# Kernel optimization log

Hardware: AMD Instinct MI355X
Metric: run time of the kernel (lower is better)

Reference implementation:

```python
import jax, jax.numpy as jnp
import numpy as np

EMBED_DIM = 768
NUM_HEADS = 12
HEAD_DIM = EMBED_DIM // NUM_HEADS
BSZ = 8
N_NODE = 512


def setup_inputs() -> dict:
    key = jax.random.key(0)
    ks = jax.random.split(key, 12)
    s = 0.02
    E = EMBED_DIM
    return {
        "query": jax.random.normal(ks[0], (N_NODE, BSZ, E), jnp.float32),
        "attention_bias": jax.random.normal(ks[1], (BSZ, NUM_HEADS, N_NODE, N_NODE), jnp.float32),
        "node_position": jax.random.normal(ks[2], (BSZ, N_NODE, 3), jnp.float32),
        "Wq": jax.random.normal(ks[3], (E, E), jnp.float32) * s,
        "bq": jnp.zeros((E,), jnp.float32),
        "Wk": jax.random.normal(ks[4], (E, E), jnp.float32) * s,
        "bk": jnp.zeros((E,), jnp.float32),
        "Wv": jax.random.normal(ks[5], (E, E), jnp.float32) * s,
        "bv": jnp.zeros((E,), jnp.float32),
        "W1": jax.random.normal(ks[6], (E, 1), jnp.float32) * s,
        "b1": jnp.zeros((1,), jnp.float32),
        "W2": jax.random.normal(ks[7], (E, 1), jnp.float32) * s,
        "b2": jnp.zeros((1,), jnp.float32),
        "W3": jax.random.normal(ks[8], (E, 1), jnp.float32) * s,
        "b3": jnp.zeros((1,), jnp.float32),
    }


def reference(query, attention_bias, node_position, Wq, bq, Wk, bk, Wv, bv,
              W1, b1, W2, b2, W3, b3):
    bsz, n = node_position.shape[:2]
    H = attention_bias.shape[1]
    E = query.shape[-1]
    hd = E // H
    scaling = hd ** -0.5

    # unit direction vectors between node pairs: delta[b,i,j] = pos[j]-pos[i]
    delta = node_position[:, None, :, :] - node_position[:, :, None, :]  # (b,n,n,3)
    dist = jnp.linalg.norm(delta, axis=-1)                               # (b,n,n)
    delta = delta / (dist[..., None] + 1e-5)

    x = jnp.swapaxes(query, 0, 1)  # (b,n,E)
    q = (x @ Wq + bq).reshape(bsz, n, H, hd).transpose(0, 2, 1, 3) * scaling  # (b,h,n,d)
    k = (x @ Wk + bk).reshape(bsz, n, H, hd).transpose(0, 2, 1, 3)
    v = (x @ Wv + bv).reshape(bsz, n, H, hd).transpose(0, 2, 1, 3)

    attn = jnp.einsum('bhid,bhjd->bhij', q, k)
    probs = jax.nn.softmax(attn + attention_bias, axis=-1)  # (b,h,i,j); dropout = identity (eval)

    # rotational aggregation: out[b,i,c,h,d] = sum_j probs[b,h,i,j]*delta[b,i,j,c]*v[b,h,j,d]
    xo = jnp.einsum('bhij,bijc,bhjd->bichd', probs, delta, v).reshape(bsz, n, 3, E)

    f1 = xo[:, :, 0, :] @ W1 + b1  # (b,n,1)
    f2 = xo[:, :, 1, :] @ W2 + b2
    f3 = xo[:, :, 2, :] @ W3 + b3
    return jnp.concatenate([f1, f2, f3], axis=-1).astype(jnp.float32)  # (b,n,3)
```

## Files before the change

kernel.cpp:

```cpp
#include <hip/hip_runtime.h>
#include <math.h>

#define EDIM 768
#define NH 12
#define HD 64
#define BSZ 8
#define NN 512
#define NCAT 1664

typedef short short8 __attribute__((ext_vector_type(8)));
typedef float f32x4 __attribute__((ext_vector_type(4)));

__device__ __forceinline__ unsigned short f2bf(float x) {
    unsigned int u = __float_as_uint(x);
    u = (u + 0x7FFF + ((u >> 16) & 1)) >> 16;
    return (unsigned short)u;
}
__device__ __forceinline__ float bf2f(unsigned short s) {
    return __uint_as_float(((unsigned int)s) << 16);
}
__device__ __forceinline__ void gl2lds16(const void* g, void* l) {
    __builtin_amdgcn_global_load_lds(
        (const __attribute__((address_space(1))) unsigned int*)g,
        (__attribute__((address_space(3))) unsigned int*)l, 16, 0, 0);
}

#define PB_GEOM_END 512
#define PB_TR_END   1664
#define PB_VW_END   1772
#define PB_CVT_END  3308
#define PB_BC_END   3315
#define PREP_BLOCKS 3350

__global__ __launch_bounds__(256) void k_prep(
        const float* __restrict__ query, const float* __restrict__ pos,
        const float* __restrict__ Wq, const float* __restrict__ bq,
        const float* __restrict__ Wk, const float* __restrict__ bk,
        const float* __restrict__ Wv, const float* __restrict__ bv,
        const float* __restrict__ W1, const float* __restrict__ W2,
        const float* __restrict__ W3,
        unsigned short* __restrict__ WT, float* __restrict__ bcat,
        unsigned short* __restrict__ Xb,
        unsigned int* __restrict__ udp) {
    __shared__ float sm[1536];
    const int bid = blockIdx.x;
    const int t = threadIdx.x;

    if (bid < PB_GEOM_END) {
        float* psx = sm; float* psy = sm + NN; float* psz = sm + 2 * NN;
        const int b = bid >> 6, i0 = (bid & 63) * 8;
        for (int idx = t; idx < NN; idx += 256) {
            const float* p = pos + ((size_t)b * NN + idx) * 3;
            psx[idx] = p[0]; psy[idx] = p[1]; psz[idx] = p[2];
        }
        __syncthreads();
        const int i = i0 + (t >> 5);
        const float qx = psx[i], qy = psy[i], qz = psz[i];
        const size_t row = ((size_t)b * NN + i) * NN;
        for (int jt = 0; jt < 4; jt++) {
            int j = ((t & 31) + jt * 32) * 4;
            unsigned int s0[4], s1[4], s2[4];
            #pragma unroll
            for (int u = 0; u < 4; u++) {
                float dx = psx[j + u] - qx, dy = psy[j + u] - qy, dz = psz[j + u] - qz;
                float inv = 1.f / (sqrtf(dx * dx + dy * dy + dz * dz) + 1e-5f);
                s0[u] = f2bf(dx * inv); s1[u] = f2bf(dy * inv); s2[u] = f2bf(dz * inv);
            }
            uint4 A = {s0[0] | (s1[0] << 16), s2[0], s0[1] | (s1[1] << 16), s2[1]};
            uint4 B = {s0[2] | (s1[2] << 16), s2[2], s0[3] | (s1[3] << 16), s2[3]};
            *(uint4*)&udp[(row + j) * 2]     = A;
            *(uint4*)&udp[(row + j) * 2 + 4] = B;
        }
    } else if (bid < PB_TR_END) {
        float (*tile)[33] = (float(*)[33])sm;
        const int tb = bid - PB_GEOM_END;
        const int n0 = (tb % 48) * 32, e0 = (tb / 48) * 32;
        const float* src = (n0 < 768) ? Wq : Wk;
        const int ol0 = (n0 < 768) ? n0 : (n0 - 768);
        const int tx = t & 31, ty = t >> 5;
        #pragma unroll
        for (int s = 0; s < 4; s++)
            tile[ty + s * 8][tx] = src[(size_t)(e0 + ty + s * 8) * EDIM + ol0 + tx];
        __syncthreads();
        #pragma unroll
        for (int s = 0; s < 4; s++)
            WT[(size_t)(n0 + ty + s * 8) * EDIM + e0 + tx] = f2bf(tile[tx][ty + s * 8]);
    } else if (bid < PB_VW_END) {
        int idx = (bid - PB_TR_END) * 256 + t;
        int o2 = idx / 768, e = idx - o2 * 768;
        int h = o2 / 3, c = o2 - (o2 / 3) * 3;
        const float* Wc = (c == 0) ? W1 : (c == 1) ? W2 : W3;
        const float4* wvp = (const float4*)(Wv + (size_t)e * EDIM + h * HD);
        const float4* wcp = (const float4*)(Wc + h * HD);
        float s = 0.f;
        #pragma unroll
        for (int d4 = 0; d4 < 16; d4++) {
            float4 a = wvp[d4], b = wcp[d4];
            s += a.x * b.x + a.y * b.y + a.z * b.z + a.w * b.w;
        }
        WT[(size_t)(1536 + o2) * EDIM + e] = f2bf(s);
    } else if (bid < PB_CVT_END) {
        int idx = (bid - PB_VW_END) * 256 + t;
        int m = idx / 96, e8 = (idx - (idx / 96) * 96) * 8;
        int b = m >> 9, i = m & (NN - 1);
        const float* src = query + ((size_t)i * BSZ + b) * EDIM + e8;
        float4 v0 = *(const float4*)src;
        float4 v1 = *(const float4*)(src + 4);
        unsigned int p0 = f2bf(v0.x) | ((unsigned int)f2bf(v0.y) << 16);
        unsigned int p1 = f2bf(v0.z) | ((unsigned int)f2bf(v0.w) << 16);
        unsigned int p2 = f2bf(v1.x) | ((unsigned int)f2bf(v1.y) << 16);
        unsigned int p3 = f2bf(v1.z) | ((unsigned int)f2bf(v1.w) << 16);
        uint4 pk = {p0, p1, p2, p3};
        *(uint4*)&Xb[(size_t)idx * 8] = pk;
    } else if (bid < PB_BC_END) {
        int o = (bid - PB_CVT_END) * 256 + t;
        if (o < NCAT) {
            float v = 0.f;
            if (o < 768) v = bq[o];
            else if (o < 1536) v = bk[o - 768];
            else if (o < 1572) {
                int o2 = o - 1536;
                int h = o2 / 3, c = o2 - (o2 / 3) * 3;
                const float* Wc = (c == 0) ? W1 : (c == 1) ? W2 : W3;
                float s = 0.f;
                for (int d = 0; d < HD; d++) s += bv[h * HD + d] * Wc[h * HD + d];
                v = s;
            }
            bcat[o] = v;
        }
    } else {
        int tid = (bid - PB_BC_END) * 256 + t;
        if (tid < 8832) {
            uint4 z = {0, 0, 0, 0};
            *(uint4*)&WT[(size_t)1572 * EDIM + (size_t)tid * 8] = z;
        }
    }
}

__global__ __launch_bounds__(256) void k_gemm_qkv(
        const unsigned short* __restrict__ Xb, const unsigned short* __restrict__ WT,
        const float* __restrict__ bcat,
        unsigned short* __restrict__ qb, unsigned short* __restrict__ kb,
        float* __restrict__ vwb) {
    __shared__ short As[8 * 64 * 8];
    __shared__ short Bs[8 * 128 * 8];
    const int t = threadIdx.x;
    const int m0 = blockIdx.x * 64, n0 = blockIdx.y * 128;
    const int w = t >> 6, lane = t & 63, quad = lane >> 4, ln = lane & 15;
    const int wm = (w & 1) * 32, wn = (w >> 1) * 64;

    f32x4 acc[2][4];
    #pragma unroll
    for (int mi = 0; mi < 2; mi++)
        #pragma unroll
        for (int ni = 0; ni < 4; ni++) acc[mi][ni] = (f32x4){0.f, 0.f, 0.f, 0.f};

    for (int k0 = 0; k0 < EDIM; k0 += 64) {
        __syncthreads();
        #pragma unroll
        for (int is = 0; is < 2; is++) {
            int slot = is * 256 + t;
            int g = slot >> 6, m = slot & 63;
            gl2lds16(Xb + (size_t)(m0 + m) * EDIM + k0 + g * 8, &As[(size_t)(is * 256 + w * 64) * 8]);
        }
        #pragma unroll
        for (int is = 0; is < 4; is++) {
            int slot = is * 256 + t;
            int g = slot >> 7, n = slot & 127;
            gl2lds16(WT + (size_t)(n0 + n) * EDIM + k0 + g * 8, &Bs[(size_t)(is * 256 + w * 64) * 8]);
        }
        __syncthreads();
        #pragma unroll
        for (int s = 0; s < 2; s++) {
            short8 af[2], bf[4];
            #pragma unroll
            for (int mi = 0; mi < 2; mi++)
                af[mi] = *(const short8*)&As[(size_t)((s * 4 + quad) * 64 + wm + mi * 16 + ln) * 8];
            #pragma unroll
            for (int ni = 0; ni < 4; ni++)
                bf[ni] = *(const short8*)&Bs[(size_t)((s * 4 + quad) * 128 + wn + ni * 16 + ln) * 8];
            #pragma unroll
            for (int mi = 0; mi < 2; mi++)
                #pragma unroll
                for (int ni = 0; ni < 4; ni++)
                    acc[mi][ni] = __builtin_amdgcn_mfma_f32_16x16x32_bf16(af[mi], bf[ni], acc[mi][ni], 0, 0, 0);
        }
    }

    #pragma unroll
    for (int mi = 0; mi < 2; mi++) {
        #pragma unroll
        for (int r = 0; r < 4; r++) {
            int mg = m0 + wm + mi * 16 + quad * 4 + r;
            int b_ = mg >> 9, i_ = mg & (NN - 1);
            #pragma unroll
            for (int ni = 0; ni < 4; ni++) {
                int o = n0 + wn + ni * 16 + ln;
                float val = acc[mi][ni][r] + bcat[o];
                if (o < 768) {
                    int h = o >> 6, d = o & 63;
                    qb[(((size_t)b_ * NH + h) * NN + i_) * HD + d] = f2bf(val * 0.125f);
                } else if (o < 1536) {
                    int o2 = o - 768;
                    int h = o2 >> 6, d = o2 & 63;
                    kb[(((size_t)b_ * NH + h) * NN + i_) * HD + d] = f2bf(val);
                } else if (o < 1572) {
                    int o2 = o - 1536;
                    int h = o2 / 3, c = o2 - (o2 / 3) * 3;
                    vwb[(((size_t)b_ * NH + h) * NN + i_) * 3 + c] = val;
                }
            }
        }
    }
}

__global__ __launch_bounds__(256, 4) void k_attn(
        const unsigned short* __restrict__ qb, const unsigned short* __restrict__ kb,
        const float* __restrict__ vwb, const float* __restrict__ bias,
        const unsigned int* __restrict__ udp,
        float* __restrict__ mp, float* __restrict__ lp,
        float* __restrict__ a0p, float* __restrict__ a1p, float* __restrict__ a2p) {
    __shared__ uint4 Qs[64 * 8];
    __shared__ uint4 Ks[128 * 8];
    __shared__ float ws0[128], ws1[128], ws2[128];

    const int t = threadIdx.x;
    const int bid = blockIdx.x;
    const int h = bid % NH;
    const int r1 = bid / NH;
    const int js = r1 & 3;
    const int it = (r1 >> 2) & 7;
    const int b = r1 >> 5;
    const int i0 = it * 64;
    const int jb = js * 128;
    const int w = t >> 6, lane = t & 63, quad = lane >> 4, ln = lane & 15;
    const size_t bh = (size_t)b * NH + h;

    const uint4* qg = (const uint4*)(qb + (bh * NN + i0) * HD);
    const uint4* kg = (const uint4*)(kb + (bh * NN + jb) * HD);
    const int rr = t >> 3, cc = t & 7;
    uint4 qv0 = qg[t];
    uint4 qv1 = qg[256 + t];
    uint4 kv0 = kg[t];
    uint4 kv1 = kg[256 + t];
    uint4 kv2 = kg[512 + t];
    uint4 kv3 = kg[768 + t];
    float wv0 = vwb[bh * (NN * 3) + (size_t)jb * 3 + t];
    float wv1 = (t < 128) ? vwb[bh * (NN * 3) + (size_t)jb * 3 + 256 + t] : 0.f;

    const float* bbase = bias + (bh * NN + i0 + w * 16 + quad * 4) * NN + jb + ln;
    f32x4 acc[8];
    #pragma unroll
    for (int jsub = 0; jsub < 8; jsub++)
        #pragma unroll
        for (int r = 0; r < 4; r++)
            acc[jsub][r] = bbase[r * NN + jsub * 16];

    const int sw = cc ^ (rr & 7);
    Qs[rr * 8 + sw] = qv0;
    Qs[(rr + 32) * 8 + sw] = qv1;
    Ks[rr * 8 + sw] = kv0;
    Ks[(rr + 32) * 8 + sw] = kv1;
    Ks[(rr + 64) * 8 + sw] = kv2;
    Ks[(rr + 96) * 8 + sw] = kv3;
    {
        int jj = t / 3, c = t - (t / 3) * 3;
        if (c == 0) ws0[jj] = wv0; else if (c == 1) ws1[jj] = wv0; else ws2[jj] = wv0;
        if (t < 128) {
            int t2 = 256 + t;
            int jj2 = t2 / 3, c2 = t2 - (t2 / 3) * 3;
            if (c2 == 0) ws0[jj2] = wv1; else if (c2 == 1) ws1[jj2] = wv1; else ws2[jj2] = wv1;
        }
    }
    __syncthreads();

    const int qrow = w * 16 + ln;
    short8 a0f = *(const short8*)&Qs[qrow * 8 + (quad ^ (qrow & 7))];
    short8 a1f = *(const short8*)&Qs[qrow * 8 + ((quad + 4) ^ (qrow & 7))];
    #pragma unroll
    for (int jsub = 0; jsub < 8; jsub++) {
        int krow = jsub * 16 + ln;
        short8 b0f = *(const short8*)&Ks[krow * 8 + (quad ^ (krow & 7))];
        short8 b1f = *(const short8*)&Ks[krow * 8 + ((quad + 4) ^ (krow & 7))];
        acc[jsub] = __builtin_amdgcn_mfma_f32_16x16x32_bf16(a0f, b0f, acc[jsub], 0, 0, 0);
        acc[jsub] = __builtin_amdgcn_mfma_f32_16x16x32_bf16(a1f, b1f, acc[jsub], 0, 0, 0);
    }

    float m_r = acc[0][0];
    #pragma unroll
    for (int jsub = 0; jsub < 8; jsub++)
        #pragma unroll
        for (int r = 0; r < 4; r++) m_r = fmaxf(m_r, acc[jsub][r]);
    #pragma unroll
    for (int off = 1; off < 64; off <<= 1) m_r = fmaxf(m_r, __shfl_xor(m_r, off, 64));

    const unsigned int* udbase = udp + (((size_t)b * NN + i0 + w * 16 + quad * 4) * NN + jb + ln) * 2;
    float lr[4] = {0.f, 0.f, 0.f, 0.f};
    float A0[4] = {0.f, 0.f, 0.f, 0.f};
    float A1[4] = {0.f, 0.f, 0.f, 0.f};
    float A2[4] = {0.f, 0.f, 0.f, 0.f};
    #pragma unroll
    for (int jsub = 0; jsub < 8; jsub++) {
        float w0 = ws0[jsub * 16 + ln];
        float w1 = ws1[jsub * 16 + ln];
        float w2 = ws2[jsub * 16 + ln];
        #pragma unroll
        for (int r = 0; r < 4; r++) {
            uint2 U = *(const uint2*)&udbase[((size_t)r * NN + jsub * 16) * 2];
            float p = __expf(acc[jsub][r] - m_r);
            lr[r] += p;
            A0[r] = fmaf(p * bf2f((unsigned short)(U.x & 0xFFFF)), w0, A0[r]);
            A1[r] = fmaf(p * bf2f((unsigned short)(U.x >> 16)), w1, A1[r]);
            A2[r] = fmaf(p * bf2f((unsigned short)(U.y & 0xFFFF)), w2, A2[r]);
        }
    }

    #pragma unroll
    for (int off = 1; off < 16; off <<= 1) {
        #pragma unroll
        for (int r = 0; r < 4; r++) {
            lr[r] += __shfl_xor(lr[r], off, 64);
            A0[r] += __shfl_xor(A0[r], off, 64);
            A1[r] += __shfl_xor(A1[r], off, 64);
            A2[r] += __shfl_xor(A2[r], off, 64);
        }
    }
    if (ln == 0) {
        #pragma unroll
        for (int r = 0; r < 4; r++) {
            int ig = i0 + w * 16 + quad * 4 + r;
            size_t o4 = (bh * NN + ig) * 4 + js;
            mp[o4] = m_r; lp[o4] = lr[r];
            a0p[o4] = A0[r]; a1p[o4] = A1[r]; a2p[o4] = A2[r];
        }
    }
}

__global__ __launch_bounds__(256) void k_finalize(
        const float* __restrict__ mp, const float* __restrict__ lp,
        const float* __restrict__ a0p, const float* __restrict__ a1p,
        const float* __restrict__ a2p,
        const float* __restrict__ b1, const float* __restrict__ b2,
        const float* __restrict__ b3, float* __restrict__ out) {
    int idx = blockIdx.x * 256 + threadIdx.x;
    int b = idx >> 9, i = idx & (NN - 1);
    float s0 = 0.f, s1 = 0.f, s2 = 0.f;
    #pragma unroll
    for (int h = 0; h < NH; h++) {
        size_t base = (((size_t)b * NH + h) * NN + i) * 4;
        f32x4 mv = *(const f32x4*)&mp[base];
        f32x4 lv = *(const f32x4*)&lp[base];
        f32x4 A0 = *(const f32x4*)&a0p[base];
        f32x4 A1 = *(const f32x4*)&a1p[base];
        f32x4 A2 = *(const f32x4*)&a2p[base];
        float M = fmaxf(fmaxf(mv[0], mv[1]), fmaxf(mv[2], mv[3]));
        float L = 0.f, c0 = 0.f, c1 = 0.f, c2 = 0.f;
        #pragma unroll
        for (int js = 0; js < 4; js++) {
            float e = __expf(mv[js] - M);
            L = fmaf(e, lv[js], L);
            c0 = fmaf(e, A0[js], c0);
            c1 = fmaf(e, A1[js], c1);
            c2 = fmaf(e, A2[js], c2);
        }
        float inv = 1.f / L;
        s0 = fmaf(c0, inv, s0);
        s1 = fmaf(c1, inv, s1);
        s2 = fmaf(c2, inv, s2);
    }
    float* op = out + (size_t)idx * 3;
    op[0] = s0 + b1[0];
    op[1] = s1 + b2[0];
    op[2] = s2 + b3[0];
}

extern "C" void kernel_launch(void* const* d_in, const int* in_sizes, int n_in,
                              void* d_out, int out_size, void* d_ws, size_t ws_size,
                              hipStream_t stream) {
    const float* query = (const float*)d_in[0];
    const float* bias  = (const float*)d_in[1];
    const float* pos   = (const float*)d_in[2];
    const float* Wq = (const float*)d_in[3];
    const float* bq = (const float*)d_in[4];
    const float* Wk = (const float*)d_in[5];
    const float* bk = (const float*)d_in[6];
    const float* Wv = (const float*)d_in[7];
    const float* bv = (const float*)d_in[8];
    const float* W1 = (const float*)d_in[9];
    const float* b1 = (const float*)d_in[10];
    const float* W2 = (const float*)d_in[11];
    const float* b2 = (const float*)d_in[12];
    const float* W3 = (const float*)d_in[13];
    const float* b3 = (const float*)d_in[14];
    float* out = (float*)d_out;

    char* p = (char*)d_ws;
    unsigned short* WT = (unsigned short*)p; p += (size_t)NCAT * EDIM * 2;
    float* bcat = (float*)p;                 p += (size_t)NCAT * 4;
    unsigned short* Xb = (unsigned short*)p; p += (size_t)BSZ * NN * EDIM * 2;
    unsigned short* qb = (unsigned short*)p; p += (size_t)BSZ * NH * NN * HD * 2;
    unsigned short* kb = (unsigned short*)p; p += (size_t)BSZ * NH * NN * HD * 2;
    float* vwb = (float*)p;                  p += (size_t)BSZ * NH * NN * 3 * 4;
    unsigned int* udp = (unsigned int*)p;    p += (size_t)BSZ * NN * NN * 8;
    const size_t PSZ = (size_t)BSZ * NH * NN * 4;
    float* mp  = (float*)p; p += PSZ * 4;
    float* lp  = (float*)p; p += PSZ * 4;
    float* a0p = (float*)p; p += PSZ * 4;
    float* a1p = (float*)p; p += PSZ * 4;
    float* a2p = (float*)p; p += PSZ * 4;

    k_prep<<<PREP_BLOCKS, 256, 0, stream>>>(query, pos, Wq, bq, Wk, bk, Wv, bv,
                                            W1, W2, W3, WT, bcat, Xb, udp);
    dim3 g2(64, 13);
    k_gemm_qkv<<<g2, 256, 0, stream>>>(Xb, WT, bcat, qb, kb, vwb);
    k_attn<<<BSZ * NH * 8 * 4, 256, 0, stream>>>(qb, kb, vwb, bias, udp,
                                                 mp, lp, a0p, a1p, a2p);
    k_finalize<<<BSZ * NN / 256, 256, 0, stream>>>(mp, lp, a0p, a1p, a2p, b1, b2, b3, out);
}
```

Baseline: 252.1 us.

## Recompute pairwise direction vectors inside attention instead of precomputing to memory

```diff
diff --git a/kernel.cpp b/kernel.cpp
--- a/kernel.cpp
+++ b/kernel.cpp
@@ -16,65 +16,34 @@
     u = (u + 0x7FFF + ((u >> 16) & 1)) >> 16;
     return (unsigned short)u;
 }
-__device__ __forceinline__ float bf2f(unsigned short s) {
-    return __uint_as_float(((unsigned int)s) << 16);
-}
 __device__ __forceinline__ void gl2lds16(const void* g, void* l) {
     __builtin_amdgcn_global_load_lds(
         (const __attribute__((address_space(1))) unsigned int*)g,
         (__attribute__((address_space(3))) unsigned int*)l, 16, 0, 0);
 }
 
-#define PB_GEOM_END 512
-#define PB_TR_END   1664
-#define PB_VW_END   1772
-#define PB_CVT_END  3308
-#define PB_BC_END   3315
-#define PREP_BLOCKS 3350
+#define PB_TR_END   1152
+#define PB_VW_END   1260
+#define PB_CVT_END  2796
+#define PB_BC_END   2803
+#define PREP_BLOCKS 2838
 
 __global__ __launch_bounds__(256) void k_prep(
-        const float* __restrict__ query, const float* __restrict__ pos,
+        const float* __restrict__ query,
         const float* __restrict__ Wq, const float* __restrict__ bq,
         const float* __restrict__ Wk, const float* __restrict__ bk,
         const float* __restrict__ Wv, const float* __restrict__ bv,
         const float* __restrict__ W1, const float* __restrict__ W2,
         const float* __restrict__ W3,
         unsigned short* __restrict__ WT, float* __restrict__ bcat,
-        unsigned short* __restrict__ Xb,
-        unsigned int* __restrict__ udp) {
+        unsigned short* __restrict__ Xb) {
     __shared__ float sm[1536];
     const int bid = blockIdx.x;
     const int t = threadIdx.x;
 
-    if (bid < PB_GEOM_END) {
-        float* psx = sm; float* psy = sm + NN; float* psz = sm + 2 * NN;
-        const int b = bid >> 6, i0 = (bid & 63) * 8;
-        for (int idx = t; idx < NN; idx += 256) {
-            const float* p = pos + ((size_t)b * NN + idx) * 3;
-            psx[idx] = p[0]; psy[idx] = p[1]; psz[idx] = p[2];
-        }
-        __syncthreads();
-        const int i = i0 + (t >> 5);
-        const float qx = psx[i], qy = psy[i], qz = psz[i];
-        const size_t row = ((size_t)b * NN + i) * NN;
-        for (int jt = 0; jt < 4; jt++) {
-            int j = ((t & 31) + jt * 32) * 4;
-            unsigned int s0[4], s1[4], s2[4];
-            #pragma unroll
-            for (int u = 0; u < 4; u++) {
-                float dx = psx[j + u] - qx, dy = psy[j + u] - qy, dz = psz[j + u] - qz;
-                float inv = 1.f / (sqrtf(dx * dx + dy * dy + dz * dz) + 1e-5f);
-                s0[u] = f2bf(dx * inv); s1[u] = f2bf(dy * inv); s2[u] = f2bf(dz * inv);
-            }
-            uint4 A = {s0[0] | (s1[0] << 16), s2[0], s0[1] | (s1[1] << 16), s2[1]};
-            uint4 B = {s0[2] | (s1[2] << 16), s2[2], s0[3] | (s1[3] << 16), s2[3]};
-            *(uint4*)&udp[(row + j) * 2]     = A;
-            *(uint4*)&udp[(row + j) * 2 + 4] = B;
-        }
-    } else if (bid < PB_TR_END) {
+    if (bid < PB_TR_END) {
         float (*tile)[33] = (float(*)[33])sm;
-        const int tb = bid - PB_GEOM_END;
-        const int n0 = (tb % 48) * 32, e0 = (tb / 48) * 32;
+        const int n0 = (bid % 48) * 32, e0 = (bid / 48) * 32;
         const float* src = (n0 < 768) ? Wq : Wk;
         const int ol0 = (n0 < 768) ? n0 : (n0 - 768);
         const int tx = t & 31, ty = t >> 5;
@@ -217,12 +186,14 @@
 __global__ __launch_bounds__(256, 4) void k_attn(
         const unsigned short* __restrict__ qb, const unsigned short* __restrict__ kb,
         const float* __restrict__ vwb, const float* __restrict__ bias,
-        const unsigned int* __restrict__ udp,
+        const float* __restrict__ pos,
         float* __restrict__ mp, float* __restrict__ lp,
         float* __restrict__ a0p, float* __restrict__ a1p, float* __restrict__ a2p) {
     __shared__ uint4 Qs[64 * 8];
     __shared__ uint4 Ks[128 * 8];
     __shared__ float ws0[128], ws1[128], ws2[128];
+    __shared__ float pjx[128], pjy[128], pjz[128];
+    __shared__ float pix[64], piy[64], piz[64];
 
     const int t = threadIdx.x;
     const int bid = blockIdx.x;
@@ -255,6 +226,17 @@
         #pragma unroll
         for (int r = 0; r < 4; r++)
             acc[jsub][r] = bbase[r * NN + jsub * 16];
+
+    for (int idx = t; idx < 384; idx += 256) {
+        float pv = pos[((size_t)b * NN + jb) * 3 + idx];
+        int jj = idx / 3, c = idx - (idx / 3) * 3;
+        if (c == 0) pjx[jj] = pv; else if (c == 1) pjy[jj] = pv; else pjz[jj] = pv;
+    }
+    if (t < 192) {
+        float pv = pos[((size_t)b * NN + i0) * 3 + t];
+        int ii = t / 3, c = t - (t / 3) * 3;
+        if (c == 0) pix[ii] = pv; else if (c == 1) piy[ii] = pv; else piz[ii] = pv;
+    }
 
     const int sw = cc ^ (rr & 7);
     Qs[rr * 8 + sw] = qv0;
@@ -294,24 +276,29 @@
     #pragma unroll
     for (int off = 1; off < 64; off <<= 1) m_r = fmaxf(m_r, __shfl_xor(m_r, off, 64));
 
-    const unsigned int* udbase = udp + (((size_t)b * NN + i0 + w * 16 + quad * 4) * NN + jb + ln) * 2;
+    const int irbase = w * 16 + quad * 4;
     float lr[4] = {0.f, 0.f, 0.f, 0.f};
     float A0[4] = {0.f, 0.f, 0.f, 0.f};
     float A1[4] = {0.f, 0.f, 0.f, 0.f};
     float A2[4] = {0.f, 0.f, 0.f, 0.f};
     #pragma unroll
     for (int jsub = 0; jsub < 8; jsub++) {
-        float w0 = ws0[jsub * 16 + ln];
-        float w1 = ws1[jsub * 16 + ln];
-        float w2 = ws2[jsub * 16 + ln];
+        const int jl = jsub * 16 + ln;
+        float w0 = ws0[jl], w1 = ws1[jl], w2 = ws2[jl];
+        float px = pjx[jl], py = pjy[jl], pz = pjz[jl];
         #pragma unroll
         for (int r = 0; r < 4; r++) {
-            uint2 U = *(const uint2*)&udbase[((size_t)r * NN + jsub * 16) * 2];
+            float dx = px - pix[irbase + r];
+            float dy = py - piy[irbase + r];
+            float dz = pz - piz[irbase + r];
+            float d2 = fmaf(dx, dx, fmaf(dy, dy, dz * dz));
+            float inv = __builtin_amdgcn_rcpf(__builtin_amdgcn_sqrtf(d2) + 1e-5f);
             float p = __expf(acc[jsub][r] - m_r);
+            float pi = p * inv;
             lr[r] += p;
-            A0[r] = fmaf(p * bf2f((unsigned short)(U.x & 0xFFFF)), w0, A0[r]);
-            A1[r] = fmaf(p * bf2f((unsigned short)(U.x >> 16)), w1, A1[r]);
-            A2[r] = fmaf(p * bf2f((unsigned short)(U.y & 0xFFFF)), w2, A2[r]);
+            A0[r] = fmaf(pi * dx, w0, A0[r]);
+            A1[r] = fmaf(pi * dy, w1, A1[r]);
+            A2[r] = fmaf(pi * dz, w2, A2[r]);
         }
     }
 
@@ -328,7 +315,7 @@
     if (ln == 0) {
         #pragma unroll
         for (int r = 0; r < 4; r++) {
-            int ig = i0 + w * 16 + quad * 4 + r;
+            int ig = i0 + irbase + r;
             size_t o4 = (bh * NN + ig) * 4 + js;
             mp[o4] = m_r; lp[o4] = lr[r];
             a0p[o4] = A0[r]; a1p[o4] = A1[r]; a2p[o4] = A2[r];
@@ -401,7 +388,6 @@
     unsigned short* qb = (unsigned short*)p; p += (size_t)BSZ * NH * NN * HD * 2;
     unsigned short* kb = (unsigned short*)p; p += (size_t)BSZ * NH * NN * HD * 2;
     float* vwb = (float*)p;                  p += (size_t)BSZ * NH * NN * 3 * 4;
-    unsigned int* udp = (unsigned int*)p;    p += (size_t)BSZ * NN * NN * 8;
     const size_t PSZ = (size_t)BSZ * NH * NN * 4;
     float* mp  = (float*)p; p += PSZ * 4;
     float* lp  = (float*)p; p += PSZ * 4;
@@ -409,11 +395,11 @@
     float* a1p = (float*)p; p += PSZ * 4;
     float* a2p = (float*)p; p += PSZ * 4;
 
-    k_prep<<<PREP_BLOCKS, 256, 0, stream>>>(query, pos, Wq, bq, Wk, bk, Wv, bv,
-                                            W1, W2, W3, WT, bcat, Xb, udp);
+    k_prep<<<PREP_BLOCKS, 256, 0, stream>>>(query, Wq, bq, Wk, bk, Wv, bv,
+                                            W1, W2, W3, WT, bcat, Xb);
     dim3 g2(64, 13);
     k_gemm_qkv<<<g2, 256, 0, stream>>>(Xb, WT, bcat, qb, kb, vwb);
-    k_attn<<<BSZ * NH * 8 * 4, 256, 0, stream>>>(qb, kb, vwb, bias, udp,
+    k_attn<<<BSZ * NH * 8 * 4, 256, 0, stream>>>(qb, kb, vwb, bias, pos,
                                                  mp, lp, a0p, a1p, a2p);
     k_finalize<<<BSZ * NN / 256, 256, 0, stream>>>(mp, lp, a0p, a1p, a2p, b1, b2, b3, out);
 }
```

Result: faster. 247.2 us (-2.0%).
